# Kernel tuning notes

Measured on AMD Instinct MI355X. Metric: run time of the kernel, lower is better.

The kernel has to match this reference:

```python
import jax, jax.numpy as jnp
import numpy as np

N = 50000   # nodes
E = 600000  # edges
D = 128     # in_feats
H = 128     # n_hidden
C = 47      # n_classes


def setup_inputs() -> dict:
    key = jax.random.key(0)
    ks = jax.random.split(key, 12)
    x = jax.random.normal(ks[0], (N, D), dtype=jnp.float32)
    src = jax.random.randint(ks[1], (E,), 0, N, dtype=jnp.int32)
    dst = jax.random.randint(ks[2], (E,), 0, N, dtype=jnp.int32)
    def lin(k, fi, fo):
        s = 1.0 / np.sqrt(fi)
        return jax.random.uniform(k, (fi, fo), jnp.float32, -s, s)
    return {
        "x": x, "src": src, "dst": dst,
        "W_self0": lin(ks[3], D, H), "W_neigh0": lin(ks[4], D, H), "b0": jnp.zeros((H,), jnp.float32),
        "W_self1": lin(ks[5], H, H), "W_neigh1": lin(ks[6], H, H), "b1": jnp.zeros((H,), jnp.float32),
        "W_self2": lin(ks[7], H, C), "W_neigh2": lin(ks[8], H, C), "b2": jnp.zeros((C,), jnp.float32),
    }


def _sage_layer(h, src, dst, W_self, W_neigh, b, act):
    # gather neighbor (src) features, mean-aggregate onto dst nodes
    msum = jax.ops.segment_sum(h[src], dst, num_segments=N)           # [N, F]
    deg = jax.ops.segment_sum(jnp.ones((src.shape[0], 1), h.dtype), dst, num_segments=N)
    h_neigh = msum / jnp.maximum(deg, 1.0)                            # zero-degree -> 0
    out = h @ W_self + h_neigh @ W_neigh + b
    return jax.nn.relu(out) if act else out


def reference(x, src, dst, W_self0, W_neigh0, b0, W_self1, W_neigh1, b1, W_self2, W_neigh2, b2):
    h = _sage_layer(x, src, dst, W_self0, W_neigh0, b0, True)
    h = _sage_layer(h, src, dst, W_self1, W_neigh1, b1, True)
    h = _sage_layer(h, src, dst, W_self2, W_neigh2, b2, False)
    return h
```

## Files before the change

### kernel.cpp

```cpp
#include <hip/hip_runtime.h>
#include <hip/hip_bf16.h>


#define THREADS 256

typedef unsigned short u16;
typedef __attribute__((ext_vector_type(8))) short bf16x8;
typedef __attribute__((ext_vector_type(4))) float f32x4;

__device__ inline u16 f2bf(float f) {
    union { float f; unsigned u; } v; v.f = f;
    unsigned r = (v.u + 0x7FFFu + ((v.u >> 16) & 1u)) >> 16;
    return (u16)r;
}
__device__ inline float bf2f(u16 b) {
    union { unsigned u; float f; } v; v.u = ((unsigned)b) << 16;
    return v.f;
}
__device__ inline unsigned pack2(float a, float b) {
    return (unsigned)f2bf(a) | ((unsigned)f2bf(b) << 16);
}

#define GLDS16(gp, lp)                                                         \
    __builtin_amdgcn_global_load_lds(                                          \
        (const __attribute__((address_space(1))) void*)(gp),                   \
        (__attribute__((address_space(3))) void*)(lp), 16, 0, 0)

__global__ void k_count(const int* __restrict__ dst, int* __restrict__ deg, int E) {
    int e = blockIdx.x * blockDim.x + threadIdx.x;
    if (e < E) atomicAdd(&deg[dst[e]], 1);
}

__global__ void k_scan_block(const int* __restrict__ deg, int* __restrict__ off,
                             int* __restrict__ bsum, int n) {
    __shared__ int s[256];
    int t = threadIdx.x;
    int base = blockIdx.x * 1024 + t * 4;
    int v[4];
#pragma unroll
    for (int i = 0; i < 4; i++) v[i] = (base + i < n) ? deg[base + i] : 0;
    int sum = v[0] + v[1] + v[2] + v[3];
    int val = sum;
    s[t] = val;
    __syncthreads();
    for (int o = 1; o < 256; o <<= 1) {
        int x = (t >= o) ? s[t - o] : 0;
        __syncthreads();
        val += x;
        s[t] = val;
        __syncthreads();
    }
    int run = val - sum;
#pragma unroll
    for (int i = 0; i < 4; i++) {
        if (base + i < n) off[base + i] = run;
        run += v[i];
    }
    if (t == 255) bsum[blockIdx.x] = val;
}

__global__ void k_scan_bsum(int* __restrict__ bsum, int nb) {
    int lane = threadIdx.x;
    int carry = 0;
    for (int start = 0; start < nb; start += 64) {
        int i = start + lane;
        int orig = (i < nb) ? bsum[i] : 0;
        int v = orig;
#pragma unroll
        for (int o = 1; o < 64; o <<= 1) {
            int u = __shfl_up(v, o, 64);
            if (lane >= o) v += u;
        }
        if (i < nb) bsum[i] = carry + v - orig;
        carry += __shfl(v, 63, 64);
    }
}

__global__ void k_scan_add(int* __restrict__ off, const int* __restrict__ bsum, int n) {
    int t = threadIdx.x;
    int base = blockIdx.x * 1024 + t * 4;
    int add = bsum[blockIdx.x];
#pragma unroll
    for (int i = 0; i < 4; i++)
        if (base + i < n) off[base + i] += add;
}

__global__ void k_fill(const int* __restrict__ src, const int* __restrict__ dst,
                       const int* __restrict__ off, int* __restrict__ cur,
                       int* __restrict__ eidx, int E) {
    int e = blockIdx.x * blockDim.x + threadIdx.x;
    if (e < E) {
        int d = dst[e];
        int p = atomicAdd(&cur[d], 1);
        eidx[off[d] + p] = src[e];
    }
}

__global__ void k_prepX(const float* __restrict__ x, u16* __restrict__ hi,
                        u16* __restrict__ lo, int n32) {
    int i = blockIdx.x * blockDim.x + threadIdx.x;
    if (i >= n32) return;
    float4 v = ((const float4*)x)[i];
    float h0 = bf2f(f2bf(v.x)), h1 = bf2f(f2bf(v.y)), h2 = bf2f(f2bf(v.z)), h3 = bf2f(f2bf(v.w));
    uint2 hp, lp;
    hp.x = pack2(h0, h1); hp.y = pack2(h2, h3);
    lp.x = pack2(v.x - h0, v.y - h1); lp.y = pack2(v.z - h2, v.w - h3);
    ((uint2*)hi)[i] = hp;
    ((uint2*)lo)[i] = lp;
}

__global__ void k_prepW3(const float* __restrict__ Ws0, const float* __restrict__ Wn0,
                         const float* __restrict__ Ws1, const float* __restrict__ Wn1,
                         const float* __restrict__ Ws2, const float* __restrict__ Wn2,
                         u16* __restrict__ Bt) {
    int idx = blockIdx.x * blockDim.x + threadIdx.x;
    if (idx >= 3 * 128 * 256) return;
    int layer = idx >> 15;
    int within = idx & 32767;
    int col = within >> 8;
    int k = within & 255;
    const float* Ws = (layer == 0) ? Ws0 : (layer == 1) ? Ws1 : Ws2;
    const float* Wn = (layer == 0) ? Wn0 : (layer == 1) ? Wn1 : Wn2;
    int fout = (layer == 2) ? 47 : 128;
    float v = 0.f;
    if (col < fout) v = (k < 128) ? Ws[k * fout + col] : Wn[(k - 128) * fout + col];
    u16 h = f2bf(v);
    Bt[layer * 65536 + within] = h;
    Bt[layer * 65536 + 32768 + within] = f2bf(v - bf2f(h));
}

__global__ void k_aggregate(const u16* __restrict__ hi_in, const int* __restrict__ eidx,
                            const int* __restrict__ off, const int* __restrict__ deg,
                            u16* __restrict__ mhi, u16* __restrict__ mlo, int n) {
    int wv = blockIdx.x * 4 + (threadIdx.x >> 6);
    int lane = threadIdx.x & 63;
    int quarter = lane >> 4;
    int ql = lane & 15;
    int node = wv * 4 + quarter;
    if (node >= n) return;
    int cnt = deg[node];
    int base = off[node];
    const uint4* h4 = (const uint4*)hi_in;
    float acc[8];
#pragma unroll
    for (int i = 0; i < 8; i++) acc[i] = 0.f;
    for (int j = 0; j < cnt; j += 8) {
        int s[8];
        float m[8];
#pragma unroll
        for (int u = 0; u < 8; u++) {
            int jj = j + u;
            s[u] = eidx[base + (jj < cnt ? jj : 0)];
            m[u] = (jj < cnt) ? 1.f : 0.f;
        }
        uint4 v[8];
#pragma unroll
        for (int u = 0; u < 8; u++) v[u] = h4[(size_t)s[u] * 16 + ql];
#pragma unroll
        for (int u = 0; u < 8; u++) {
            acc[0] = fmaf(m[u], bf2f((u16)(v[u].x & 0xffffu)), acc[0]);
            acc[1] = fmaf(m[u], bf2f((u16)(v[u].x >> 16)), acc[1]);
            acc[2] = fmaf(m[u], bf2f((u16)(v[u].y & 0xffffu)), acc[2]);
            acc[3] = fmaf(m[u], bf2f((u16)(v[u].y >> 16)), acc[3]);
            acc[4] = fmaf(m[u], bf2f((u16)(v[u].z & 0xffffu)), acc[4]);
            acc[5] = fmaf(m[u], bf2f((u16)(v[u].z >> 16)), acc[5]);
            acc[6] = fmaf(m[u], bf2f((u16)(v[u].w & 0xffffu)), acc[6]);
            acc[7] = fmaf(m[u], bf2f((u16)(v[u].w >> 16)), acc[7]);
        }
    }
    float iv = 1.0f / (float)(cnt > 1 ? cnt : 1);
    float a[8], r[8];
#pragma unroll
    for (int i = 0; i < 8; i++) {
        a[i] = acc[i] * iv;
        r[i] = bf2f(f2bf(a[i]));
    }
    uint4 hp, lp;
    hp.x = pack2(a[0], a[1]); hp.y = pack2(a[2], a[3]);
    hp.z = pack2(a[4], a[5]); hp.w = pack2(a[6], a[7]);
    lp.x = pack2(a[0] - r[0], a[1] - r[1]); lp.y = pack2(a[2] - r[2], a[3] - r[3]);
    lp.z = pack2(a[4] - r[4], a[5] - r[5]); lp.w = pack2(a[6] - r[6], a[7] - r[7]);
    ((uint4*)mhi)[(size_t)node * 16 + ql] = hp;
    ((uint4*)mlo)[(size_t)node * 16 + ql] = lp;
}

__global__ __launch_bounds__(256) void k_gemm_mfma(
    const u16* __restrict__ Ahi_s, const u16* __restrict__ Alo_s,
    const u16* __restrict__ Ahi_n, const u16* __restrict__ Alo_n,
    const u16* __restrict__ Bthi, const u16* __restrict__ Btlo,
    const float* __restrict__ bias, float* __restrict__ out_f32,
    u16* __restrict__ out_hi, u16* __restrict__ out_lo, int n, int fout, int relu) {
    __shared__ u16 sAhi[64 * 32];
    __shared__ u16 sAlo[64 * 32];
    __shared__ u16 sBhi[128 * 32];
    __shared__ u16 sBlo[128 * 32];

    int t = threadIdx.x;
    int w = t >> 6;
    int lane = t & 63;
    int wr = w >> 1, wc = w & 1;
    size_t row0 = (size_t)blockIdx.x * 64;

    f32x4 acc[2][4];
#pragma unroll
    for (int r = 0; r < 2; r++)
#pragma unroll
        for (int c = 0; c < 4; c++) acc[r][c] = (f32x4){0.f, 0.f, 0.f, 0.f};

    for (int kk = 0; kk < 256; kk += 32) {
        const u16* Phi = (kk < 128) ? Ahi_s : Ahi_n;
        const u16* Plo = (kk < 128) ? Alo_s : Alo_n;
        int kc = kk & 127;
        __syncthreads();
        {
            int r = w * 16 + (lane >> 2);
            int cb = (lane & 3) * 8;
            GLDS16(Phi + (row0 + r) * 128 + kc + cb, &sAhi[r * 32 + cb]);
            GLDS16(Plo + (row0 + r) * 128 + kc + cb, &sAlo[r * 32 + cb]);
        }
#pragma unroll
        for (int i = 0; i < 2; i++) {
            int c = w * 32 + i * 16 + (lane >> 2);
            int cb = (lane & 3) * 8;
            GLDS16(Bthi + (size_t)c * 256 + kk + cb, &sBhi[c * 32 + cb]);
            GLDS16(Btlo + (size_t)c * 256 + kk + cb, &sBlo[c * 32 + cb]);
        }
        __syncthreads();

        bf16x8 a_hi[2], a_lo[2], b_hi[4], b_lo[4];
        int q8 = (lane >> 4) * 8;
#pragma unroll
        for (int r = 0; r < 2; r++) {
            int ad = (wr * 32 + r * 16 + (lane & 15)) * 32 + q8;
            a_hi[r] = *(const bf16x8*)&sAhi[ad];
            a_lo[r] = *(const bf16x8*)&sAlo[ad];
        }
#pragma unroll
        for (int c = 0; c < 4; c++) {
            int ad = (wc * 64 + c * 16 + (lane & 15)) * 32 + q8;
            b_hi[c] = *(const bf16x8*)&sBhi[ad];
            b_lo[c] = *(const bf16x8*)&sBlo[ad];
        }
#pragma unroll
        for (int r = 0; r < 2; r++)
#pragma unroll
            for (int c = 0; c < 4; c++) {
                acc[r][c] = __builtin_amdgcn_mfma_f32_16x16x32_bf16(
                    a_hi[r], b_hi[c], acc[r][c], 0, 0, 0);
                acc[r][c] = __builtin_amdgcn_mfma_f32_16x16x32_bf16(
                    a_hi[r], b_lo[c], acc[r][c], 0, 0, 0);
                acc[r][c] = __builtin_amdgcn_mfma_f32_16x16x32_bf16(
                    a_lo[r], b_hi[c], acc[r][c], 0, 0, 0);
            }
    }

    int quad = lane >> 4;
    int lcol = lane & 15;
#pragma unroll
    for (int r = 0; r < 2; r++) {
#pragma unroll
        for (int c = 0; c < 4; c++) {
            int col = wc * 64 + c * 16 + lcol;
            float bv = (col < fout) ? bias[col] : 0.f;
#pragma unroll
            for (int g = 0; g < 4; g++) {
                size_t row = row0 + wr * 32 + r * 16 + quad * 4 + g;
                if (row >= (size_t)n || col >= fout) continue;
                float v = acc[r][c][g] + bv;
                if (relu) v = v > 0.f ? v : 0.f;
                if (out_f32) out_f32[row * fout + col] = v;
                if (out_hi) {
                    u16 h = f2bf(v);
                    out_hi[row * 128 + col] = h;
                    out_lo[row * 128 + col] = f2bf(v - bf2f(h));
                }
            }
        }
    }
}

extern "C" void kernel_launch(void* const* d_in, const int* in_sizes, int n_in,
                              void* d_out, int out_size, void* d_ws, size_t ws_size,
                              hipStream_t stream) {
    const float* x = (const float*)d_in[0];
    const int* src = (const int*)d_in[1];
    const int* dst = (const int*)d_in[2];
    const float* Ws0 = (const float*)d_in[3];
    const float* Wn0 = (const float*)d_in[4];
    const float* b0 = (const float*)d_in[5];
    const float* Ws1 = (const float*)d_in[6];
    const float* Wn1 = (const float*)d_in[7];
    const float* b1 = (const float*)d_in[8];
    const float* Ws2 = (const float*)d_in[9];
    const float* Wn2 = (const float*)d_in[10];
    const float* b2 = (const float*)d_in[11];
    float* out = (float*)d_out;

    const int N = in_sizes[0] / 128;
    const int E = in_sizes[1];
    const int Npad = ((N + 63) / 64) * 64;

    char* p = (char*)d_ws;
    u16* P0hi = (u16*)p; p += (size_t)Npad * 128 * 2;
    u16* P0lo = (u16*)p; p += (size_t)Npad * 128 * 2;
    u16* P1hi = (u16*)p; p += (size_t)Npad * 128 * 2;
    u16* P1lo = (u16*)p; p += (size_t)Npad * 128 * 2;
    u16* Mhi = (u16*)p; p += (size_t)Npad * 128 * 2;
    u16* Mlo = (u16*)p; p += (size_t)Npad * 128 * 2;
    u16* Bt = (u16*)p; p += 3 * 2 * 128 * 256 * 2;
    int* deg = (int*)p; p += (size_t)N * 4;
    int* cur = (int*)p; p += (size_t)N * 4;
    int* off = (int*)p; p += (size_t)N * 4;
    int* eidx = (int*)p; p += (size_t)E * 4;
    int* bsum = (int*)p;

    const int nbE = (E + THREADS - 1) / THREADS;
    const int nbScan = (N + 1023) / 1024;
    const int nbAgg = (N + 15) / 16;
    const int nbGemm = (N + 63) / 64;
    const int nbPX = (N * 32 + THREADS - 1) / THREADS;
    const int nbPW = (3 * 128 * 256 + THREADS - 1) / THREADS;

    hipMemsetAsync(deg, 0, (size_t)2 * N * sizeof(int), stream);

    k_count<<<nbE, THREADS, 0, stream>>>(dst, deg, E);
    k_scan_block<<<nbScan, 256, 0, stream>>>(deg, off, bsum, N);
    k_scan_bsum<<<1, 64, 0, stream>>>(bsum, nbScan);
    k_scan_add<<<nbScan, 256, 0, stream>>>(off, bsum, N);
    k_fill<<<nbE, THREADS, 0, stream>>>(src, dst, off, cur, eidx, E);

    k_prepX<<<nbPX, THREADS, 0, stream>>>(x, P0hi, P0lo, N * 32);
    k_prepW3<<<nbPW, THREADS, 0, stream>>>(Ws0, Wn0, Ws1, Wn1, Ws2, Wn2, Bt);

    k_aggregate<<<nbAgg, 256, 0, stream>>>(P0hi, eidx, off, deg, Mhi, Mlo, N);
    k_gemm_mfma<<<nbGemm, 256, 0, stream>>>(P0hi, P0lo, Mhi, Mlo,
                                            Bt + 0 * 65536, Bt + 0 * 65536 + 32768, b0,
                                            (float*)nullptr, P1hi, P1lo, N, 128, 1);
    k_aggregate<<<nbAgg, 256, 0, stream>>>(P1hi, eidx, off, deg, Mhi, Mlo, N);
    k_gemm_mfma<<<nbGemm, 256, 0, stream>>>(P1hi, P1lo, Mhi, Mlo,
                                            Bt + 1 * 65536, Bt + 1 * 65536 + 32768, b1,
                                            (float*)nullptr, P0hi, P0lo, N, 128, 1);
    k_aggregate<<<nbAgg, 256, 0, stream>>>(P0hi, eidx, off, deg, Mhi, Mlo, N);
    k_gemm_mfma<<<nbGemm, 256, 0, stream>>>(P0hi, P0lo, Mhi, Mlo,
                                            Bt + 2 * 65536, Bt + 2 * 65536 + 32768, b2,
                                            out, (u16*)nullptr, (u16*)nullptr, N, 47, 0);
}
```

Before: 309.3 us.

## Merge preamble kernels, fold block-sum scan into add, slim final-layer GEMM

Fuses degree counting, X hi/lo splitting and weight packing into one preamble kernel. It also removes the single-wave block-sum scan by having each scan_add block reduce the preceding block sums itself. Together these cut the number of launches and serial dependencies. For the last layer (fout <= 64), each wave now covers 16 rows by 64 columns, so MFMA work on the padded output columns is skipped. The cost is some redundant reads of the block sums and divergent branches inside the merged kernel.

```diff
diff --git a/kernel.cpp b/kernel.cpp
--- a/kernel.cpp
+++ b/kernel.cpp
@@ -26,9 +26,38 @@
         (const __attribute__((address_space(1))) void*)(gp),                   \
         (__attribute__((address_space(3))) void*)(lp), 16, 0, 0)
 
-__global__ void k_count(const int* __restrict__ dst, int* __restrict__ deg, int E) {
-    int e = blockIdx.x * blockDim.x + threadIdx.x;
-    if (e < E) atomicAdd(&deg[dst[e]], 1);
+__global__ void k_preamble(const float* __restrict__ x, u16* __restrict__ hi,
+                           u16* __restrict__ lo, int n32,
+                           const int* __restrict__ dst, int* __restrict__ deg, int E,
+                           const float* __restrict__ Ws0, const float* __restrict__ Wn0,
+                           const float* __restrict__ Ws1, const float* __restrict__ Wn1,
+                           const float* __restrict__ Ws2, const float* __restrict__ Wn2,
+                           u16* __restrict__ Bt) {
+    int idx = blockIdx.x * blockDim.x + threadIdx.x;
+    if (idx < n32) {
+        float4 v = ((const float4*)x)[idx];
+        float h0 = bf2f(f2bf(v.x)), h1 = bf2f(f2bf(v.y)), h2 = bf2f(f2bf(v.z)), h3 = bf2f(f2bf(v.w));
+        uint2 hp, lp;
+        hp.x = pack2(h0, h1); hp.y = pack2(h2, h3);
+        lp.x = pack2(v.x - h0, v.y - h1); lp.y = pack2(v.z - h2, v.w - h3);
+        ((uint2*)hi)[idx] = hp;
+        ((uint2*)lo)[idx] = lp;
+    }
+    if (idx < E) atomicAdd(&deg[dst[idx]], 1);
+    if (idx < 3 * 128 * 256) {
+        int layer = idx >> 15;
+        int within = idx & 32767;
+        int col = within >> 8;
+        int k = within & 255;
+        const float* Ws = (layer == 0) ? Ws0 : (layer == 1) ? Ws1 : Ws2;
+        const float* Wn = (layer == 0) ? Wn0 : (layer == 1) ? Wn1 : Wn2;
+        int fout = (layer == 2) ? 47 : 128;
+        float v = 0.f;
+        if (col < fout) v = (k < 128) ? Ws[k * fout + col] : Wn[(k - 128) * fout + col];
+        u16 h = f2bf(v);
+        Bt[layer * 65536 + within] = h;
+        Bt[layer * 65536 + 32768 + within] = f2bf(v - bf2f(h));
+    }
 }
 
 __global__ void k_scan_block(const int* __restrict__ deg, int* __restrict__ off,
@@ -59,27 +88,19 @@
     if (t == 255) bsum[blockIdx.x] = val;
 }
 
-__global__ void k_scan_bsum(int* __restrict__ bsum, int nb) {
-    int lane = threadIdx.x;
-    int carry = 0;
-    for (int start = 0; start < nb; start += 64) {
-        int i = start + lane;
-        int orig = (i < nb) ? bsum[i] : 0;
-        int v = orig;
-#pragma unroll
-        for (int o = 1; o < 64; o <<= 1) {
-            int u = __shfl_up(v, o, 64);
-            if (lane >= o) v += u;
-        }
-        if (i < nb) bsum[i] = carry + v - orig;
-        carry += __shfl(v, 63, 64);
-    }
-}
-
 __global__ void k_scan_add(int* __restrict__ off, const int* __restrict__ bsum, int n) {
+    __shared__ int sAdd;
     int t = threadIdx.x;
+    if (t < 64) {
+        int v = 0;
+        for (int i = t; i < blockIdx.x; i += 64) v += bsum[i];
+#pragma unroll
+        for (int o = 32; o; o >>= 1) v += __shfl_xor(v, o, 64);
+        if (t == 0) sAdd = v;
+    }
+    __syncthreads();
+    int add = sAdd;
     int base = blockIdx.x * 1024 + t * 4;
-    int add = bsum[blockIdx.x];
 #pragma unroll
     for (int i = 0; i < 4; i++)
         if (base + i < n) off[base + i] += add;
@@ -94,39 +115,6 @@
         int p = atomicAdd(&cur[d], 1);
         eidx[off[d] + p] = src[e];
     }
-}
-
-__global__ void k_prepX(const float* __restrict__ x, u16* __restrict__ hi,
-                        u16* __restrict__ lo, int n32) {
-    int i = blockIdx.x * blockDim.x + threadIdx.x;
-    if (i >= n32) return;
-    float4 v = ((const float4*)x)[i];
-    float h0 = bf2f(f2bf(v.x)), h1 = bf2f(f2bf(v.y)), h2 = bf2f(f2bf(v.z)), h3 = bf2f(f2bf(v.w));
-    uint2 hp, lp;
-    hp.x = pack2(h0, h1); hp.y = pack2(h2, h3);
-    lp.x = pack2(v.x - h0, v.y - h1); lp.y = pack2(v.z - h2, v.w - h3);
-    ((uint2*)hi)[i] = hp;
-    ((uint2*)lo)[i] = lp;
-}
-
-__global__ void k_prepW3(const float* __restrict__ Ws0, const float* __restrict__ Wn0,
-                         const float* __restrict__ Ws1, const float* __restrict__ Wn1,
-                         const float* __restrict__ Ws2, const float* __restrict__ Wn2,
-                         u16* __restrict__ Bt) {
-    int idx = blockIdx.x * blockDim.x + threadIdx.x;
-    if (idx >= 3 * 128 * 256) return;
-    int layer = idx >> 15;
-    int within = idx & 32767;
-    int col = within >> 8;
-    int k = within & 255;
-    const float* Ws = (layer == 0) ? Ws0 : (layer == 1) ? Ws1 : Ws2;
-    const float* Wn = (layer == 0) ? Wn0 : (layer == 1) ? Wn1 : Wn2;
-    int fout = (layer == 2) ? 47 : 128;
-    float v = 0.f;
-    if (col < fout) v = (k < 128) ? Ws[k * fout + col] : Wn[(k - 128) * fout + col];
-    u16 h = f2bf(v);
-    Bt[layer * 65536 + within] = h;
-    Bt[layer * 65536 + 32768 + within] = f2bf(v - bf2f(h));
 }
 
 __global__ void k_aggregate(const u16* __restrict__ hi_in, const int* __restrict__ eidx,
@@ -201,6 +189,11 @@
     int wr = w >> 1, wc = w & 1;
     size_t row0 = (size_t)blockIdx.x * 64;
 
+    const bool slim = (fout <= 64);
+    const int rbase = slim ? (w * 16) : (wr * 32);
+    const int nR = slim ? 1 : 2;
+    const int cbase = slim ? 0 : (wc * 64);
+
     f32x4 acc[2][4];
 #pragma unroll
     for (int r = 0; r < 2; r++)
@@ -231,18 +224,20 @@
         int q8 = (lane >> 4) * 8;
 #pragma unroll
         for (int r = 0; r < 2; r++) {
-            int ad = (wr * 32 + r * 16 + (lane & 15)) * 32 + q8;
+            if (r >= nR) continue;
+            int ad = (rbase + r * 16 + (lane & 15)) * 32 + q8;
             a_hi[r] = *(const bf16x8*)&sAhi[ad];
             a_lo[r] = *(const bf16x8*)&sAlo[ad];
         }
 #pragma unroll
         for (int c = 0; c < 4; c++) {
-            int ad = (wc * 64 + c * 16 + (lane & 15)) * 32 + q8;
+            int ad = (cbase + c * 16 + (lane & 15)) * 32 + q8;
             b_hi[c] = *(const bf16x8*)&sBhi[ad];
             b_lo[c] = *(const bf16x8*)&sBlo[ad];
         }
 #pragma unroll
-        for (int r = 0; r < 2; r++)
+        for (int r = 0; r < 2; r++) {
+            if (r >= nR) continue;
 #pragma unroll
             for (int c = 0; c < 4; c++) {
                 acc[r][c] = __builtin_amdgcn_mfma_f32_16x16x32_bf16(
@@ -252,19 +247,21 @@
                 acc[r][c] = __builtin_amdgcn_mfma_f32_16x16x32_bf16(
                     a_lo[r], b_hi[c], acc[r][c], 0, 0, 0);
             }
+        }
     }
 
     int quad = lane >> 4;
     int lcol = lane & 15;
 #pragma unroll
     for (int r = 0; r < 2; r++) {
+        if (r >= nR) continue;
 #pragma unroll
         for (int c = 0; c < 4; c++) {
-            int col = wc * 64 + c * 16 + lcol;
+            int col = cbase + c * 16 + lcol;
             float bv = (col < fout) ? bias[col] : 0.f;
 #pragma unroll
             for (int g = 0; g < 4; g++) {
-                size_t row = row0 + wr * 32 + r * 16 + quad * 4 + g;
+                size_t row = row0 + rbase + r * 16 + quad * 4 + g;
                 if (row >= (size_t)n || col >= fout) continue;
                 float v = acc[r][c][g] + bv;
                 if (relu) v = v > 0.f ? v : 0.f;
@@ -314,23 +311,23 @@
     int* eidx = (int*)p; p += (size_t)E * 4;
     int* bsum = (int*)p;
 
+    const int nPX = N * 32;
+    int nPre = nPX;
+    if (E > nPre) nPre = E;
+    if (3 * 128 * 256 > nPre) nPre = 3 * 128 * 256;
+    const int nbPre = (nPre + THREADS - 1) / THREADS;
     const int nbE = (E + THREADS - 1) / THREADS;
     const int nbScan = (N + 1023) / 1024;
     const int nbAgg = (N + 15) / 16;
     const int nbGemm = (N + 63) / 64;
-    const int nbPX = (N * 32 + THREADS - 1) / THREADS;
-    const int nbPW = (3 * 128 * 256 + THREADS - 1) / THREADS;
 
     hipMemsetAsync(deg, 0, (size_t)2 * N * sizeof(int), stream);
 
-    k_count<<<nbE, THREADS, 0, stream>>>(dst, deg, E);
+    k_preamble<<<nbPre, THREADS, 0, stream>>>(x, P0hi, P0lo, nPX, dst, deg, E,
+                                              Ws0, Wn0, Ws1, Wn1, Ws2, Wn2, Bt);
     k_scan_block<<<nbScan, 256, 0, stream>>>(deg, off, bsum, N);
-    k_scan_bsum<<<1, 64, 0, stream>>>(bsum, nbScan);
     k_scan_add<<<nbScan, 256, 0, stream>>>(off, bsum, N);
     k_fill<<<nbE, THREADS, 0, stream>>>(src, dst, off, cur, eidx, E);
-
-    k_prepX<<<nbPX, THREADS, 0, stream>>>(x, P0hi, P0lo, N * 32);
-    k_prepW3<<<nbPW, THREADS, 0, stream>>>(Ws0, Wn0, Ws1, Wn1, Ws2, Wn2, Bt);
 
     k_aggregate<<<nbAgg, 256, 0, stream>>>(P0hi, eidx, off, deg, Mhi, Mlo, N);
     k_gemm_mfma<<<nbGemm, 256, 0, stream>>>(P0hi, P0lo, Mhi, Mlo,
```

Result: faster. 299.0 us (-3.3%).
